# Optimization experiments

Hardware: AMD Instinct MI355X
Metric: run time of the kernel (lower is better)

## Reference

```python
import jax, jax.numpy as jnp
import numpy as np
from jax import lax

N_SAMPLES = 64
POS_PER_BATCH = 16  # round(64 * 0.25)
POS_IOU = 0.5
EXCL_IOU = 0.1
IMG_H = 1024.0
IMG_W = 1024.0
BBOX_STD = jnp.array([0.1, 0.1, 0.2, 0.2], dtype=jnp.float32)
EPS = 1e-7


def _iou_matrix(rois, gts):
    # rois (R,4), gts (G,4) in (y1,x1,y2,x2) -> (R,G)
    y1 = jnp.maximum(rois[:, None, 0], gts[None, :, 0])
    x1 = jnp.maximum(rois[:, None, 1], gts[None, :, 1])
    y2 = jnp.minimum(rois[:, None, 2], gts[None, :, 2])
    x2 = jnp.minimum(rois[:, None, 3], gts[None, :, 3])
    inter = jnp.clip(y2 - y1, 0.0) * jnp.clip(x2 - x1, 0.0)
    area_r = jnp.clip(rois[:, 2] - rois[:, 0], 0.0) * jnp.clip(rois[:, 3] - rois[:, 1], 0.0)
    area_g = jnp.clip(gts[:, 2] - gts[:, 0], 0.0) * jnp.clip(gts[:, 3] - gts[:, 1], 0.0)
    union = area_r[:, None] + area_g[None, :] - inter
    return inter / jnp.maximum(union, EPS)


def _get_offsets(rois, gts):
    rh = jnp.maximum(rois[:, 2] - rois[:, 0], EPS)
    rw = jnp.maximum(rois[:, 3] - rois[:, 1], EPS)
    rcy = rois[:, 0] + 0.5 * rh
    rcx = rois[:, 1] + 0.5 * rw
    gh = jnp.maximum(gts[:, 2] - gts[:, 0], EPS)
    gw = jnp.maximum(gts[:, 3] - gts[:, 1], EPS)
    gcy = gts[:, 0] + 0.5 * gh
    gcx = gts[:, 1] + 0.5 * gw
    return jnp.stack([(gcy - rcy) / rh, (gcx - rcx) / rw,
                      jnp.log(gh / rh), jnp.log(gw / rw)], axis=-1)


def _per_image(roi, gt_bbox_n, gt_label):
    # roi (R,4) normalized; gt_bbox_n (G,4) normalized; gt_label (G,)
    roi_valid = jnp.any(roi != 0, axis=1)
    gt_valid = jnp.any(gt_bbox_n != 0, axis=1)
    ious = _iou_matrix(roi, gt_bbox_n)           # (R,G)
    ious = jnp.where(gt_valid[None, :], ious, -1.0)
    max_iou = ious.max(axis=1)
    idx_max_gt = ious.argmax(axis=1)

    pos = roi_valid & (max_iou >= POS_IOU)
    neg = roi_valid & (max_iou < POS_IOU) & (max_iou >= EXCL_IOU)
    R = roi.shape[0]
    ar = jnp.arange(R)
    # deterministic subsample (lowest index first) in place of tf.random_shuffle
    _, pos_idx = lax.top_k(jnp.where(pos, R - ar, 0), POS_PER_BATCH)
    _, neg_idx = lax.top_k(jnp.where(neg, R - ar, 0), N_SAMPLES)
    n_pos = jnp.minimum(pos.sum(), POS_PER_BATCH)
    n_neg = jnp.minimum(neg.sum(), N_SAMPLES - n_pos)

    slots = jnp.arange(N_SAMPLES)
    is_pos = slots < n_pos
    is_neg = (slots >= n_pos) & (slots < n_pos + n_neg)
    valid = is_pos | is_neg
    pidx = pos_idx[jnp.clip(slots, 0, POS_PER_BATCH - 1)]
    nidx = neg_idx[jnp.clip(slots - n_pos, 0, N_SAMPLES - 1)]
    ridx = jnp.where(is_pos, pidx, jnp.where(is_neg, nidx, 0))

    s_roi_raw = roi[ridx]                        # (64,4)
    gidx = idx_max_gt[ridx]
    s_gt = gt_bbox_n[gidx]
    vf = valid.astype(roi.dtype)[:, None]
    s_roi = s_roi_raw * vf
    s_off = (_get_offsets(s_roi_raw, s_gt) * vf) / BBOX_STD
    s_lab = jnp.where(is_pos, gt_label[gidx], 0).astype(jnp.int32)
    return s_roi, s_off, s_lab


def _forward(normalized_rois, gt_bboxes, gt_labels):
    gt_norm = gt_bboxes / jnp.array([IMG_H, IMG_W, IMG_H, IMG_W], dtype=gt_bboxes.dtype)
    return jax.vmap(_per_image)(normalized_rois, gt_norm, gt_labels)


def setup_inputs() -> dict:
    key = jax.random.key(0)
    k1, k2, k3, k4, k5, k6 = jax.random.split(key, 6)
    B, R, G = 8, 20000, 256
    cy = jax.random.uniform(k1, (B, G)) * IMG_H
    cx = jax.random.uniform(k2, (B, G)) * IMG_W
    sz = jax.random.uniform(k3, (B, G, 2)) * 180.0 + 20.0
    y1 = jnp.clip(cy - 0.5 * sz[..., 0], 0, IMG_H)
    y2 = jnp.clip(cy + 0.5 * sz[..., 0], 0, IMG_H)
    x1 = jnp.clip(cx - 0.5 * sz[..., 1], 0, IMG_W)
    x2 = jnp.clip(cx + 0.5 * sz[..., 1], 0, IMG_W)
    gt_bboxes = jnp.stack([y1, x1, y2, x2], axis=-1).astype(jnp.float32)
    gt_labels = jax.random.randint(k4, (B, G), 1, 81, dtype=jnp.int32)
    gt_norm = gt_bboxes / jnp.array([IMG_H, IMG_W, IMG_H, IMG_W], dtype=jnp.float32)
    # jittered copies of gt boxes guarantee positive RoIs
    jit = jnp.clip(jnp.tile(gt_norm, (1, 4, 1)) + 0.02 * jax.random.normal(k5, (B, 4 * G, 4)), 0.0, 1.0)
    rc = jax.random.uniform(k6, (B, R - 4 * G, 4))
    ry1 = jnp.minimum(rc[..., 0], rc[..., 2]); ry2 = jnp.maximum(rc[..., 0], rc[..., 2])
    rx1 = jnp.minimum(rc[..., 1], rc[..., 3]); rx2 = jnp.maximum(rc[..., 1], rc[..., 3])
    rand_rois = jnp.stack([ry1, rx1, ry2, rx2], axis=-1)
    normalized_rois = jnp.concatenate([jit, rand_rois], axis=1).astype(jnp.float32)
    return {"normalized_rois": normalized_rois, "gt_bboxes": gt_bboxes, "gt_labels": gt_labels}


def reference(normalized_rois, gt_bboxes, gt_labels):
    return _forward(normalized_rois, gt_bboxes, gt_labels)
```

## Files before the change

kernel.cpp:

```cpp
#include <hip/hip_runtime.h>

#pragma clang fp contract(off)

#define GMAX 256

__device__ __forceinline__ unsigned int ordf(float f) {
    unsigned int u = __float_as_uint(f);
    return (u & 0x80000000u) ? ~u : (u | 0x80000000u);
}

__global__ __launch_bounds__(256) void iou_cls_kernel(
    const float* __restrict__ rois, const float* __restrict__ gts,
    unsigned long long* __restrict__ pmask, unsigned long long* __restrict__ nmask,
    int R, int G, int NW)
{
    const int bi    = blockIdx.y;
    const int lane  = threadIdx.x & 63;
    const int gbase = threadIdx.x & 192;
    const int r     = blockIdx.x * 64 + lane;

    __shared__ float4 gbox[GMAX];
    __shared__ float  garea[GMAX];
    __shared__ unsigned long long bp[4], ba[4];

    for (int t = threadIdx.x; t < GMAX; t += 256) {
        float a = 4.f, b = 4.f, c = 4.f, d = 4.f, area = 0.f;
        if (t < G) {
            const float4 g4 = *reinterpret_cast<const float4*>(gts + ((size_t)bi * G + t) * 4);
            const float s = 1.0f / 1024.0f;
            const float na = g4.x * s, nb = g4.y * s, nc = g4.z * s, nd = g4.w * s;
            if ((na != 0.f) || (nb != 0.f) || (nc != 0.f) || (nd != 0.f)) {
                a = na; b = nb; c = nc; d = nd;
                area = fmaxf(nc - na, 0.f) * fmaxf(nd - nb, 0.f);
            }
        }
        gbox[t]  = make_float4(a, b, c, d);
        garea[t] = area;
    }
    __syncthreads();

    float4 rr = make_float4(0.f, 0.f, 0.f, 0.f);
    if (r < R) rr = *reinterpret_cast<const float4*>(rois + ((size_t)bi * R + r) * 4);
    const bool rv = (r < R) &&
        ((rr.x != 0.f) || (rr.y != 0.f) || (rr.z != 0.f) || (rr.w != 0.f));
    const float ar = fmaxf(rr.z - rr.x, 0.f) * fmaxf(rr.w - rr.y, 0.f);

    const double C1 = 33554431.0 / 67108864.0;
    const double C2 = 26843545.0 / 268435456.0;
    bool anyp = false, any1 = false;

    #pragma unroll 4
    for (int j = 0; j < 64; ++j) {
        const int g = gbase + j;
        const float4 gb = gbox[g];
        const float y1 = fmaxf(rr.x, gb.x);
        const float x1 = fmaxf(rr.y, gb.y);
        const float y2 = fminf(rr.z, gb.z);
        const float x2 = fminf(rr.w, gb.w);
        const float inter = fmaxf(y2 - y1, 0.f) * fmaxf(x2 - x1, 0.f);
        const float uni   = (ar + garea[g]) - inter;
        const float uni2  = fmaxf(uni, 1e-7f);
        const double A = (double)inter;
        const double B = (double)uni2;
        anyp = anyp | (A >= C1 * B);
        any1 = any1 | (A >  C2 * B);
    }

    const int wave = threadIdx.x >> 6;
    const unsigned long long brv = __ballot(rv);
    bp[wave] = __ballot(anyp);
    ba[wave] = __ballot(any1);
    __syncthreads();

    if (threadIdx.x == 0) {
        const unsigned long long por = bp[0] | bp[1] | bp[2] | bp[3];
        const unsigned long long aor = ba[0] | ba[1] | ba[2] | ba[3];
        pmask[(size_t)bi * NW + blockIdx.x] = brv & por;
        nmask[(size_t)bi * NW + blockIdx.x] = brv & aor & ~por;
    }
}

__global__ __launch_bounds__(512) void select_kernel(
    const float* __restrict__ rois, const float* __restrict__ gts,
    const int* __restrict__ labels,
    const unsigned long long* __restrict__ pmask, const unsigned long long* __restrict__ nmask,
    float* __restrict__ out, int R, int G, int B, int NW)
{
    const int bi  = blockIdx.x;
    const int tid = threadIdx.x;

    __shared__ int sp[512], sn[512];
    __shared__ float4 sgt[GMAX];
    __shared__ float  sgv[GMAX];
    __shared__ int plist[16], nlist[64];
    __shared__ int sridx[64];
    __shared__ unsigned long long skey[64];

    for (int t = tid; t < G; t += 512) {
        const float4 g4 = *reinterpret_cast<const float4*>(gts + ((size_t)bi * G + t) * 4);
        const float s = 1.0f / 1024.0f;
        const float a = g4.x * s, b = g4.y * s, c = g4.z * s, d = g4.w * s;
        sgt[t] = make_float4(a, b, c, d);
        sgv[t] = ((a != 0.f) || (b != 0.f) || (c != 0.f) || (d != 0.f)) ? 1.0f : 0.0f;
    }

    unsigned long long mp = 0ull, mn = 0ull;
    if (tid < NW) {
        mp = pmask[(size_t)bi * NW + tid];
        mn = nmask[(size_t)bi * NW + tid];
    }
    const int cp = __popcll(mp);
    const int cn = __popcll(mn);
    sp[tid] = cp; sn[tid] = cn;
    if (tid < 16) plist[tid] = 0;
    if (tid < 64) nlist[tid] = 0;
    __syncthreads();
    for (int off = 1; off < 512; off <<= 1) {
        const int vp = (tid >= off) ? sp[tid - off] : 0;
        const int vn = (tid >= off) ? sn[tid - off] : 0;
        __syncthreads();
        sp[tid] += vp; sn[tid] += vn;
        __syncthreads();
    }
    const int basep = sp[tid] - cp;
    const int basen = sn[tid] - cn;

    if (mp && basep < 16) {
        int rank = basep; unsigned long long m = mp;
        while (m && rank < 16) { const int b = __ffsll(m) - 1; plist[rank++] = tid * 64 + b; m &= m - 1; }
    }
    if (mn && basen < 64) {
        int rank = basen; unsigned long long m = mn;
        while (m && rank < 64) { const int b = __ffsll(m) - 1; nlist[rank++] = tid * 64 + b; m &= m - 1; }
    }
    __syncthreads();

    const int tot_p = sp[511];
    const int tot_n = sn[511];
    const int n_pos = min(tot_p, 16);
    const int n_neg = min(tot_n, 64 - n_pos);

    if (tid < 64) {
        const int slot = tid;
        const bool isp = slot < n_pos;
        const bool isn = (!isp) && (slot < n_pos + n_neg);
        sridx[slot] = isp ? plist[slot] : (isn ? nlist[slot - n_pos] : 0);
        skey[slot]  = 0ull;
    }
    __syncthreads();

    {
        const int slot = tid >> 3;
        const int sub  = tid & 7;
        const int ridx = sridx[slot];
        const float4 rr = *reinterpret_cast<const float4*>(rois + ((size_t)bi * R + ridx) * 4);
        const float ar = fmaxf(rr.z - rr.x, 0.f) * fmaxf(rr.w - rr.y, 0.f);
        float best = -1.0f;
        int bidx = sub * 32;
        for (int j = 0; j < 32; ++j) {
            const int g = sub * 32 + j;
            if (g >= G) break;
            const float4 gb = sgt[g];
            const float y1 = fmaxf(rr.x, gb.x);
            const float x1 = fmaxf(rr.y, gb.y);
            const float y2 = fminf(rr.z, gb.z);
            const float x2 = fminf(rr.w, gb.w);
            const float inter = fmaxf(y2 - y1, 0.f) * fmaxf(x2 - x1, 0.f);
            const float ga = fmaxf(gb.z - gb.x, 0.f) * fmaxf(gb.w - gb.y, 0.f);
            const float uni = (ar + ga) - inter;
            float v = inter / fmaxf(uni, 1e-7f);
            if (sgv[g] == 0.0f) v = -1.0f;
            if (v > best) { best = v; bidx = g; }
        }
        const unsigned long long key =
            ((unsigned long long)ordf(best) << 32) | (unsigned int)(~(unsigned int)bidx);
        atomicMax(&skey[slot], key);
    }
    __syncthreads();

    if (tid < 64) {
        const int slot = tid;
        const bool isp = slot < n_pos;
        const bool isn = (!isp) && (slot < n_pos + n_neg);
        const int ridx = sridx[slot];
        const int gidx = (int)(~(unsigned int)(skey[slot] & 0xFFFFFFFFull));

        const float4 rr = *reinterpret_cast<const float4*>(rois + ((size_t)bi * R + ridx) * 4);
        const float4 gb = sgt[gidx];
        const float vf = (isp || isn) ? 1.0f : 0.0f;
        const float eps = 1e-7f;

        const float rh  = fmaxf(rr.z - rr.x, eps);
        const float rw  = fmaxf(rr.w - rr.y, eps);
        const float rcy = rr.x + 0.5f * rh;
        const float rcx = rr.y + 0.5f * rw;
        const float gh  = fmaxf(gb.z - gb.x, eps);
        const float gw  = fmaxf(gb.w - gb.y, eps);
        const float gcy = gb.x + 0.5f * gh;
        const float gcx = gb.y + 0.5f * gw;

        float o0 = (gcy - rcy) / rh;
        float o1 = (gcx - rcx) / rw;
        float o2 = logf(gh / rh);
        float o3 = logf(gw / rw);
        o0 = (o0 * vf) / 0.1f;
        o1 = (o1 * vf) / 0.1f;
        o2 = (o2 * vf) / 0.2f;
        o3 = (o3 * vf) / 0.2f;

        const int base = bi * 64 + slot;
        reinterpret_cast<float4*>(out)[base] = make_float4(rr.x * vf, rr.y * vf, rr.z * vf, rr.w * vf);
        reinterpret_cast<float4*>(out + (size_t)B * 256)[base] = make_float4(o0, o1, o2, o3);
        out[(size_t)B * 512 + base] = isp ? (float)labels[(size_t)bi * G + gidx] : 0.0f;
    }
}

extern "C" void kernel_launch(void* const* d_in, const int* in_sizes, int n_in,
                              void* d_out, int out_size, void* d_ws, size_t ws_size,
                              hipStream_t stream)
{
    const float* rois   = (const float*)d_in[0];
    const float* gts    = (const float*)d_in[1];
    const int*   labels = (const int*)d_in[2];
    float* out = (float*)d_out;

    const int B = out_size / 576;
    const int G = in_sizes[2] / B;
    const int R = in_sizes[0] / (4 * B);
    const int NW = (R + 63) / 64;

    unsigned long long* pmask = (unsigned long long*)d_ws;
    unsigned long long* nmask = pmask + (size_t)B * NW;

    dim3 gridA(NW, B);
    iou_cls_kernel<<<gridA, 256, 0, stream>>>(rois, gts, pmask, nmask, R, G, NW);
    select_kernel<<<B, 512, 0, stream>>>(rois, gts, labels, pmask, nmask, out, R, G, B, NW);
}
```

Measured before the change: 97.85 us.

## Fuse IoU classification and selection into one kernel via last-block atomic counter

Merges the two kernels into one. The last block to finish for each image, found with an atomic counter and release/acquire fences, does the prefix scan, sampling and target computation. That block reuses the gt boxes already in shared memory and replaces the 512-thread shared-memory scan with a wave-shuffle scan over packed counts. This removes one kernel launch and the separate select pass, but adds a hipMemsetAsync for the counters and serializes the tail work onto whichever block arrives last.

```diff
diff --git a/kernel.cpp b/kernel.cpp
--- a/kernel.cpp
+++ b/kernel.cpp
@@ -9,21 +9,25 @@
     return (u & 0x80000000u) ? ~u : (u | 0x80000000u);
 }
 
-__global__ __launch_bounds__(256) void iou_cls_kernel(
+__global__ __launch_bounds__(256) void fused_kernel(
     const float* __restrict__ rois, const float* __restrict__ gts,
+    const int* __restrict__ labels,
     unsigned long long* __restrict__ pmask, unsigned long long* __restrict__ nmask,
-    int R, int G, int NW)
+    int* __restrict__ counters,
+    float* __restrict__ out, int R, int G, int B, int NW)
 {
-    const int bi    = blockIdx.y;
-    const int lane  = threadIdx.x & 63;
-    const int gbase = threadIdx.x & 192;
-    const int r     = blockIdx.x * 64 + lane;
+    const int bi   = blockIdx.y;
+    const int tid  = threadIdx.x;
+    const int lane = tid & 63;
+    const int wave = tid >> 6;
+    const int r    = blockIdx.x * 64 + lane;
 
     __shared__ float4 gbox[GMAX];
     __shared__ float  garea[GMAX];
-    __shared__ unsigned long long bp[4], ba[4];
-
-    for (int t = threadIdx.x; t < GMAX; t += 256) {
+    __shared__ unsigned long long bp4[4], ba4[4];
+    __shared__ int lastflag;
+
+    for (int t = tid; t < GMAX; t += 256) {
         float a = 4.f, b = 4.f, c = 4.f, d = 4.f, area = 0.f;
         if (t < G) {
             const float4 g4 = *reinterpret_cast<const float4*>(gts + ((size_t)bi * G + t) * 4);
@@ -49,127 +53,127 @@
     const double C2 = 26843545.0 / 268435456.0;
     bool anyp = false, any1 = false;
 
-    #pragma unroll 4
-    for (int j = 0; j < 64; ++j) {
-        const int g = gbase + j;
-        const float4 gb = gbox[g];
-        const float y1 = fmaxf(rr.x, gb.x);
-        const float x1 = fmaxf(rr.y, gb.y);
-        const float y2 = fminf(rr.z, gb.z);
-        const float x2 = fminf(rr.w, gb.w);
-        const float inter = fmaxf(y2 - y1, 0.f) * fmaxf(x2 - x1, 0.f);
-        const float uni   = (ar + garea[g]) - inter;
-        const float uni2  = fmaxf(uni, 1e-7f);
-        const double A = (double)inter;
-        const double B = (double)uni2;
-        anyp = anyp | (A >= C1 * B);
-        any1 = any1 | (A >  C2 * B);
-    }
-
-    const int wave = threadIdx.x >> 6;
-    const unsigned long long brv = __ballot(rv);
-    bp[wave] = __ballot(anyp);
-    ba[wave] = __ballot(any1);
-    __syncthreads();
-
-    if (threadIdx.x == 0) {
-        const unsigned long long por = bp[0] | bp[1] | bp[2] | bp[3];
-        const unsigned long long aor = ba[0] | ba[1] | ba[2] | ba[3];
-        pmask[(size_t)bi * NW + blockIdx.x] = brv & por;
-        nmask[(size_t)bi * NW + blockIdx.x] = brv & aor & ~por;
-    }
-}
-
-__global__ __launch_bounds__(512) void select_kernel(
-    const float* __restrict__ rois, const float* __restrict__ gts,
-    const int* __restrict__ labels,
-    const unsigned long long* __restrict__ pmask, const unsigned long long* __restrict__ nmask,
-    float* __restrict__ out, int R, int G, int B, int NW)
-{
-    const int bi  = blockIdx.x;
-    const int tid = threadIdx.x;
-
-    __shared__ int sp[512], sn[512];
-    __shared__ float4 sgt[GMAX];
-    __shared__ float  sgv[GMAX];
-    __shared__ int plist[16], nlist[64];
-    __shared__ int sridx[64];
-    __shared__ unsigned long long skey[64];
-
-    for (int t = tid; t < G; t += 512) {
-        const float4 g4 = *reinterpret_cast<const float4*>(gts + ((size_t)bi * G + t) * 4);
-        const float s = 1.0f / 1024.0f;
-        const float a = g4.x * s, b = g4.y * s, c = g4.z * s, d = g4.w * s;
-        sgt[t] = make_float4(a, b, c, d);
-        sgv[t] = ((a != 0.f) || (b != 0.f) || (c != 0.f) || (d != 0.f)) ? 1.0f : 0.0f;
-    }
-
-    unsigned long long mp = 0ull, mn = 0ull;
-    if (tid < NW) {
-        mp = pmask[(size_t)bi * NW + tid];
-        mn = nmask[(size_t)bi * NW + tid];
-    }
-    const int cp = __popcll(mp);
-    const int cn = __popcll(mn);
-    sp[tid] = cp; sn[tid] = cn;
-    if (tid < 16) plist[tid] = 0;
-    if (tid < 64) nlist[tid] = 0;
-    __syncthreads();
-    for (int off = 1; off < 512; off <<= 1) {
-        const int vp = (tid >= off) ? sp[tid - off] : 0;
-        const int vn = (tid >= off) ? sn[tid - off] : 0;
-        __syncthreads();
-        sp[tid] += vp; sn[tid] += vn;
-        __syncthreads();
-    }
-    const int basep = sp[tid] - cp;
-    const int basen = sn[tid] - cn;
-
-    if (mp && basep < 16) {
-        int rank = basep; unsigned long long m = mp;
-        while (m && rank < 16) { const int b = __ffsll(m) - 1; plist[rank++] = tid * 64 + b; m &= m - 1; }
-    }
-    if (mn && basen < 64) {
-        int rank = basen; unsigned long long m = mn;
-        while (m && rank < 64) { const int b = __ffsll(m) - 1; nlist[rank++] = tid * 64 + b; m &= m - 1; }
-    }
-    __syncthreads();
-
-    const int tot_p = sp[511];
-    const int tot_n = sn[511];
-    const int n_pos = min(tot_p, 16);
-    const int n_neg = min(tot_n, 64 - n_pos);
-
-    if (tid < 64) {
-        const int slot = tid;
-        const bool isp = slot < n_pos;
-        const bool isn = (!isp) && (slot < n_pos + n_neg);
-        sridx[slot] = isp ? plist[slot] : (isn ? nlist[slot - n_pos] : 0);
-        skey[slot]  = 0ull;
-    }
-    __syncthreads();
-
     {
-        const int slot = tid >> 3;
-        const int sub  = tid & 7;
-        const int ridx = sridx[slot];
-        const float4 rr = *reinterpret_cast<const float4*>(rois + ((size_t)bi * R + ridx) * 4);
-        const float ar = fmaxf(rr.z - rr.x, 0.f) * fmaxf(rr.w - rr.y, 0.f);
-        float best = -1.0f;
-        int bidx = sub * 32;
-        for (int j = 0; j < 32; ++j) {
-            const int g = sub * 32 + j;
-            if (g >= G) break;
-            const float4 gb = sgt[g];
+        const int gbase = wave << 6;
+        #pragma unroll 4
+        for (int j = 0; j < 64; ++j) {
+            const int g = gbase + j;
+            const float4 gb = gbox[g];
             const float y1 = fmaxf(rr.x, gb.x);
             const float x1 = fmaxf(rr.y, gb.y);
             const float y2 = fminf(rr.z, gb.z);
             const float x2 = fminf(rr.w, gb.w);
             const float inter = fmaxf(y2 - y1, 0.f) * fmaxf(x2 - x1, 0.f);
-            const float ga = fmaxf(gb.z - gb.x, 0.f) * fmaxf(gb.w - gb.y, 0.f);
-            const float uni = (ar + ga) - inter;
+            const float uni   = (ar + garea[g]) - inter;
+            const double A  = (double)inter;
+            const double Bd = (double)fmaxf(uni, 1e-7f);
+            anyp = anyp | (A >= C1 * Bd);
+            any1 = any1 | (A >  C2 * Bd);
+        }
+    }
+
+    const unsigned long long brv = __ballot(rv);
+    bp4[wave] = __ballot(anyp);
+    ba4[wave] = __ballot(any1);
+    __syncthreads();
+
+    if (tid == 0) {
+        const unsigned long long por = bp4[0] | bp4[1] | bp4[2] | bp4[3];
+        const unsigned long long aor = ba4[0] | ba4[1] | ba4[2] | ba4[3];
+        __hip_atomic_store(&pmask[(size_t)bi * NW + blockIdx.x], brv & por,
+                           __ATOMIC_RELAXED, __HIP_MEMORY_SCOPE_AGENT);
+        __hip_atomic_store(&nmask[(size_t)bi * NW + blockIdx.x], brv & aor & ~por,
+                           __ATOMIC_RELAXED, __HIP_MEMORY_SCOPE_AGENT);
+        __builtin_amdgcn_fence(__ATOMIC_RELEASE, "agent");
+        const int old = __hip_atomic_fetch_add(&counters[bi], 1,
+                           __ATOMIC_RELAXED, __HIP_MEMORY_SCOPE_AGENT);
+        lastflag = (old == NW - 1) ? 1 : 0;
+    }
+    __syncthreads();
+    if (!lastflag) return;
+
+    __builtin_amdgcn_fence(__ATOMIC_ACQUIRE, "agent");
+
+    const unsigned long long* pm = pmask + (size_t)bi * NW;
+    const unsigned long long* nm = nmask + (size_t)bi * NW;
+    const int w0 = 2 * tid, w1 = 2 * tid + 1;
+    unsigned long long mp0 = 0, mp1 = 0, mn0 = 0, mn1 = 0;
+    if (w0 < NW) {
+        mp0 = __hip_atomic_load(&pm[w0], __ATOMIC_RELAXED, __HIP_MEMORY_SCOPE_AGENT);
+        mn0 = __hip_atomic_load(&nm[w0], __ATOMIC_RELAXED, __HIP_MEMORY_SCOPE_AGENT);
+    }
+    if (w1 < NW) {
+        mp1 = __hip_atomic_load(&pm[w1], __ATOMIC_RELAXED, __HIP_MEMORY_SCOPE_AGENT);
+        mn1 = __hip_atomic_load(&nm[w1], __ATOMIC_RELAXED, __HIP_MEMORY_SCOPE_AGENT);
+    }
+    const int cp0 = __popcll(mp0), cp1 = __popcll(mp1);
+    const int cn0 = __popcll(mn0), cn1 = __popcll(mn1);
+
+    int packed = ((cp0 + cp1) << 16) | (cn0 + cn1);
+    int incl = packed;
+    #pragma unroll
+    for (int d = 1; d < 64; d <<= 1) {
+        const int v = __shfl_up(incl, d, 64);
+        if (lane >= d) incl += v;
+    }
+    __shared__ int wsum[4];
+    if (lane == 63) wsum[wave] = incl;
+    __syncthreads();
+    int wpre = 0;
+    #pragma unroll
+    for (int wv = 0; wv < 4; ++wv) if (wv < wave) wpre += wsum[wv];
+    incl += wpre;
+    const int excl = incl - packed;
+    const int tot  = wsum[0] + wsum[1] + wsum[2] + wsum[3];
+    const int totp = tot >> 16;
+    const int totn = tot & 0xFFFF;
+
+    __shared__ int plist[16], nlist[64];
+    {
+        int rank = excl >> 16;
+        unsigned long long m = mp0;
+        while (m && rank < 16) { const int b = __ffsll(m) - 1; plist[rank++] = w0 * 64 + b; m &= m - 1; }
+        rank = (excl >> 16) + cp0; m = mp1;
+        while (m && rank < 16) { const int b = __ffsll(m) - 1; plist[rank++] = w1 * 64 + b; m &= m - 1; }
+        rank = excl & 0xFFFF; m = mn0;
+        while (m && rank < 64) { const int b = __ffsll(m) - 1; nlist[rank++] = w0 * 64 + b; m &= m - 1; }
+        rank = (excl & 0xFFFF) + cn0; m = mn1;
+        while (m && rank < 64) { const int b = __ffsll(m) - 1; nlist[rank++] = w1 * 64 + b; m &= m - 1; }
+    }
+    __syncthreads();
+
+    const int n_pos = min(totp, 16);
+    const int n_neg = min(totn, 64 - n_pos);
+
+    __shared__ int sridx[64];
+    __shared__ unsigned long long skey[64];
+    if (tid < 64) {
+        const bool isp = tid < n_pos;
+        const bool isn = (!isp) && (tid < n_pos + n_neg);
+        sridx[tid] = isp ? plist[tid] : (isn ? nlist[tid - n_pos] : 0);
+        skey[tid]  = 0ull;
+    }
+    __syncthreads();
+
+    {
+        const int slot = tid >> 2;
+        const int sub  = tid & 3;
+        const int ridx = sridx[slot];
+        const float4 rb = *reinterpret_cast<const float4*>(rois + ((size_t)bi * R + ridx) * 4);
+        const float arb = fmaxf(rb.z - rb.x, 0.f) * fmaxf(rb.w - rb.y, 0.f);
+        float best = -1.0f;
+        int bidx = sub * 64;
+        for (int j = 0; j < 64; ++j) {
+            const int g = sub * 64 + j;
+            const float4 gb = gbox[g];
+            const float y1 = fmaxf(rb.x, gb.x);
+            const float x1 = fmaxf(rb.y, gb.y);
+            const float y2 = fminf(rb.z, gb.z);
+            const float x2 = fminf(rb.w, gb.w);
+            const float inter = fmaxf(y2 - y1, 0.f) * fmaxf(x2 - x1, 0.f);
+            const float uni = (arb + garea[g]) - inter;
             float v = inter / fmaxf(uni, 1e-7f);
-            if (sgv[g] == 0.0f) v = -1.0f;
+            if (gb.x == 4.f) v = -1.0f;
             if (v > best) { best = v; bidx = g; }
         }
         const unsigned long long key =
@@ -185,15 +189,15 @@
         const int ridx = sridx[slot];
         const int gidx = (int)(~(unsigned int)(skey[slot] & 0xFFFFFFFFull));
 
-        const float4 rr = *reinterpret_cast<const float4*>(rois + ((size_t)bi * R + ridx) * 4);
-        const float4 gb = sgt[gidx];
+        const float4 rb = *reinterpret_cast<const float4*>(rois + ((size_t)bi * R + ridx) * 4);
+        const float4 gb = gbox[gidx];
         const float vf = (isp || isn) ? 1.0f : 0.0f;
         const float eps = 1e-7f;
 
-        const float rh  = fmaxf(rr.z - rr.x, eps);
-        const float rw  = fmaxf(rr.w - rr.y, eps);
-        const float rcy = rr.x + 0.5f * rh;
-        const float rcx = rr.y + 0.5f * rw;
+        const float rh  = fmaxf(rb.z - rb.x, eps);
+        const float rw  = fmaxf(rb.w - rb.y, eps);
+        const float rcy = rb.x + 0.5f * rh;
+        const float rcx = rb.y + 0.5f * rw;
         const float gh  = fmaxf(gb.z - gb.x, eps);
         const float gw  = fmaxf(gb.w - gb.y, eps);
         const float gcy = gb.x + 0.5f * gh;
@@ -209,7 +213,7 @@
         o3 = (o3 * vf) / 0.2f;
 
         const int base = bi * 64 + slot;
-        reinterpret_cast<float4*>(out)[base] = make_float4(rr.x * vf, rr.y * vf, rr.z * vf, rr.w * vf);
+        reinterpret_cast<float4*>(out)[base] = make_float4(rb.x * vf, rb.y * vf, rb.z * vf, rb.w * vf);
         reinterpret_cast<float4*>(out + (size_t)B * 256)[base] = make_float4(o0, o1, o2, o3);
         out[(size_t)B * 512 + base] = isp ? (float)labels[(size_t)bi * G + gidx] : 0.0f;
     }
@@ -231,8 +235,10 @@
 
     unsigned long long* pmask = (unsigned long long*)d_ws;
     unsigned long long* nmask = pmask + (size_t)B * NW;
-
-    dim3 gridA(NW, B);
-    iou_cls_kernel<<<gridA, 256, 0, stream>>>(rois, gts, pmask, nmask, R, G, NW);
-    select_kernel<<<B, 512, 0, stream>>>(rois, gts, labels, pmask, nmask, out, R, G, B, NW);
+    int* counters = (int*)(nmask + (size_t)B * NW);
+
+    (void)hipMemsetAsync(counters, 0, (size_t)B * sizeof(int), stream);
+    dim3 grid(NW, B);
+    fused_kernel<<<grid, 256, 0, stream>>>(rois, gts, labels, pmask, nmask,
+                                           counters, out, R, G, B, NW);
 }
```

Result: slower. 124.1 us (+26.9%).
